# Optimization experiments

Measured on AMD Instinct MI355X. Metric: run time of the kernel, lower is better.

The kernel has to match this reference:

```python
import jax, jax.numpy as jnp
import numpy as np

# grid_size buffer registered in __init__: [1, gx, gy, gz]
GRID = jnp.array([1.0, 0.1, 0.1, 0.1], dtype=jnp.float32)


def setup_inputs() -> dict:
    key = jax.random.key(0)
    k1, k2 = jax.random.split(key)
    N, B = 4_000_000, 8
    batch = jax.random.randint(k1, (N, 1), 0, B).astype(jnp.float32)
    xyz = jax.random.uniform(k2, (N, 3), minval=0.0, maxval=50.0)
    points = jnp.concatenate([batch, xyz], axis=1)  # [N, 4]
    return {"points": points}


def reference(points):
    N = points.shape[0]
    # bounding box (batch column padded by 0.5 so each integer batch id gets its own bin)
    start = points.min(axis=0).at[0].add(-0.5)  # [4]
    end = points.max(axis=0).at[0].add(0.5)     # [4]
    # per-dim voxel coordinates and linear cluster id (grid_cluster)
    coords = jnp.floor((points - start) / GRID).astype(jnp.int32)        # [N, 4]
    num_vox = jnp.floor((end - start) / GRID).astype(jnp.int32) + 1      # [4]
    strides = jnp.concatenate([jnp.ones((1,), jnp.int32), jnp.cumprod(num_vox[:-1])])
    cluster = (coords * strides).sum(axis=1)                             # [N] int32
    # sorted unique + inverse; pad to static size N for jit-compatibility
    _, inv = jnp.unique(cluster, size=N, fill_value=jnp.int32(-1), return_inverse=True)
    inv = inv.reshape(N)
    # scatter-mean of points into voxels (rows >= num_grids are zero padding)
    sums = jax.ops.segment_sum(points, inv, num_segments=N)              # [N, 4]
    counts = jax.ops.segment_sum(jnp.ones((N,), points.dtype), inv, num_segments=N)
    sampled_grids = sums / jnp.maximum(counts, 1.0)[:, None]
    return sampled_grids, inv
```

## Files before the change

kernel.cpp:

```cpp
#include <hip/hip_runtime.h>
#include <stdint.h>


#define BSHIFT   17
#define BVOX     (1u << BSHIFT)
#define BWORDS   (BVOX / 32)
#define NBUCK    8800u
#define UCAP     640
#define NBLK     512
#define MMBLK    512
#define GRID_B   1.0f
#define GRID_XYZ 0.1f

static inline size_t alignUp(size_t x, size_t a) { return (x + a - 1) & ~(a - 1); }

struct DerivedT { float s0, s1, s2, s3; int st1, st2, st3; };

__device__ __forceinline__ DerivedT derive(const float* mm) {
    DerivedT d;
    d.s0 = mm[0] - 0.5f; d.s1 = mm[1]; d.s2 = mm[2]; d.s3 = mm[3];
    float e0 = mm[4] + 0.5f;
    int nv0 = (int)floorf((e0    - d.s0) / GRID_B)   + 1;
    int nv1 = (int)floorf((mm[5] - d.s1) / GRID_XYZ) + 1;
    int nv2 = (int)floorf((mm[6] - d.s2) / GRID_XYZ) + 1;
    d.st1 = nv0; d.st2 = nv0 * nv1; d.st3 = nv0 * nv1 * nv2;
    return d;
}

__device__ __forceinline__ uint32_t clusterOf(float4 p, const DerivedT& d) {
    int c0 = (int)floorf((p.x - d.s0) / GRID_B);
    int c1 = (int)floorf((p.y - d.s1) / GRID_XYZ);
    int c2 = (int)floorf((p.z - d.s2) / GRID_XYZ);
    int c3 = (int)floorf((p.w - d.s3) / GRID_XYZ);
    uint32_t c = (uint32_t)(c0 + c1 * d.st1 + c2 * d.st2 + c3 * d.st3);
    const uint32_t cap = NBUCK * BVOX - 1u;
    return (c < cap) ? c : cap;
}

__global__ __launch_bounds__(256) void k_minmax_partial(const float4* __restrict__ pts, int n,
                                                        float* __restrict__ partial) {
    __shared__ float smn[4][4], smx[4][4];
    float mn0 = 3.4e38f, mn1 = 3.4e38f, mn2 = 3.4e38f, mn3 = 3.4e38f;
    float mx0 = -3.4e38f, mx1 = -3.4e38f, mx2 = -3.4e38f, mx3 = -3.4e38f;
    for (int i = blockIdx.x * blockDim.x + threadIdx.x; i < n; i += gridDim.x * blockDim.x) {
        float4 p = pts[i];
        mn0 = fminf(mn0, p.x); mx0 = fmaxf(mx0, p.x);
        mn1 = fminf(mn1, p.y); mx1 = fmaxf(mx1, p.y);
        mn2 = fminf(mn2, p.z); mx2 = fmaxf(mx2, p.z);
        mn3 = fminf(mn3, p.w); mx3 = fmaxf(mx3, p.w);
    }
    #pragma unroll
    for (int off = 32; off >= 1; off >>= 1) {
        mn0 = fminf(mn0, __shfl_xor(mn0, off)); mx0 = fmaxf(mx0, __shfl_xor(mx0, off));
        mn1 = fminf(mn1, __shfl_xor(mn1, off)); mx1 = fmaxf(mx1, __shfl_xor(mx1, off));
        mn2 = fminf(mn2, __shfl_xor(mn2, off)); mx2 = fmaxf(mx2, __shfl_xor(mx2, off));
        mn3 = fminf(mn3, __shfl_xor(mn3, off)); mx3 = fmaxf(mx3, __shfl_xor(mx3, off));
    }
    const int wave = threadIdx.x >> 6;
    if ((threadIdx.x & 63) == 0) {
        smn[wave][0] = mn0; smn[wave][1] = mn1; smn[wave][2] = mn2; smn[wave][3] = mn3;
        smx[wave][0] = mx0; smx[wave][1] = mx1; smx[wave][2] = mx2; smx[wave][3] = mx3;
    }
    __syncthreads();
    if (threadIdx.x == 0) {
        #pragma unroll
        for (int w = 1; w < 4; ++w) {
            smn[0][0] = fminf(smn[0][0], smn[w][0]); smx[0][0] = fmaxf(smx[0][0], smx[w][0]);
            smn[0][1] = fminf(smn[0][1], smn[w][1]); smx[0][1] = fmaxf(smx[0][1], smx[w][1]);
            smn[0][2] = fminf(smn[0][2], smn[w][2]); smx[0][2] = fmaxf(smx[0][2], smx[w][2]);
            smn[0][3] = fminf(smn[0][3], smn[w][3]); smx[0][3] = fmaxf(smx[0][3], smx[w][3]);
        }
        float* p = partial + (size_t)blockIdx.x * 8;
        p[0] = smn[0][0]; p[1] = smn[0][1]; p[2] = smn[0][2]; p[3] = smn[0][3];
        p[4] = smx[0][0]; p[5] = smx[0][1]; p[6] = smx[0][2]; p[7] = smx[0][3];
    }
}

__global__ __launch_bounds__(256) void k_minmax_final(const float* __restrict__ partial,
                                                      float* __restrict__ mm) {
    __shared__ float smn[4][4], smx[4][4];
    float mn0 = 3.4e38f, mn1 = 3.4e38f, mn2 = 3.4e38f, mn3 = 3.4e38f;
    float mx0 = -3.4e38f, mx1 = -3.4e38f, mx2 = -3.4e38f, mx3 = -3.4e38f;
    for (int b = threadIdx.x; b < MMBLK; b += 256) {
        const float* p = partial + (size_t)b * 8;
        mn0 = fminf(mn0, p[0]); mn1 = fminf(mn1, p[1]);
        mn2 = fminf(mn2, p[2]); mn3 = fminf(mn3, p[3]);
        mx0 = fmaxf(mx0, p[4]); mx1 = fmaxf(mx1, p[5]);
        mx2 = fmaxf(mx2, p[6]); mx3 = fmaxf(mx3, p[7]);
    }
    #pragma unroll
    for (int off = 32; off >= 1; off >>= 1) {
        mn0 = fminf(mn0, __shfl_xor(mn0, off)); mx0 = fmaxf(mx0, __shfl_xor(mx0, off));
        mn1 = fminf(mn1, __shfl_xor(mn1, off)); mx1 = fmaxf(mx1, __shfl_xor(mx1, off));
        mn2 = fminf(mn2, __shfl_xor(mn2, off)); mx2 = fmaxf(mx2, __shfl_xor(mx2, off));
        mn3 = fminf(mn3, __shfl_xor(mn3, off)); mx3 = fmaxf(mx3, __shfl_xor(mx3, off));
    }
    const int wave = threadIdx.x >> 6;
    if ((threadIdx.x & 63) == 0) {
        smn[wave][0] = mn0; smn[wave][1] = mn1; smn[wave][2] = mn2; smn[wave][3] = mn3;
        smx[wave][0] = mx0; smx[wave][1] = mx1; smx[wave][2] = mx2; smx[wave][3] = mx3;
    }
    __syncthreads();
    if (threadIdx.x == 0) {
        #pragma unroll
        for (int w = 1; w < 4; ++w) {
            smn[0][0] = fminf(smn[0][0], smn[w][0]); smx[0][0] = fmaxf(smx[0][0], smx[w][0]);
            smn[0][1] = fminf(smn[0][1], smn[w][1]); smx[0][1] = fmaxf(smx[0][1], smx[w][1]);
            smn[0][2] = fminf(smn[0][2], smn[w][2]); smx[0][2] = fmaxf(smx[0][2], smx[w][2]);
            smn[0][3] = fminf(smn[0][3], smn[w][3]); smx[0][3] = fmaxf(smx[0][3], smx[w][3]);
        }
        mm[0] = smn[0][0]; mm[1] = smn[0][1]; mm[2] = smn[0][2]; mm[3] = smn[0][3];
        mm[4] = smx[0][0]; mm[5] = smx[0][1]; mm[6] = smx[0][2]; mm[7] = smx[0][3];
    }
}

__global__ __launch_bounds__(256) void k_hist(const float4* __restrict__ pts, int n, int ch,
                                              const float* __restrict__ mm,
                                              uint32_t* __restrict__ hist) {
    __shared__ uint32_t h[NBUCK];
    DerivedT d = derive(mm);
    const int blk = blockIdx.x, t = threadIdx.x;
    for (int i = t; i < (int)NBUCK; i += 256) h[i] = 0;
    __syncthreads();
    const int s = blk * ch, e = min(n, s + ch);
    for (int i = s + t; i < e; i += 256) {
        uint32_t c = clusterOf(pts[i], d);
        atomicAdd(&h[c >> BSHIFT], 1u);
    }
    __syncthreads();
    uint32_t* row = hist + (size_t)blk * NBUCK;
    for (int i = t; i < (int)NBUCK; i += 256) row[i] = h[i];
}

__global__ __launch_bounds__(256) void k_total(const uint32_t* __restrict__ hist,
                                               uint32_t* __restrict__ tot) {
    int b = blockIdx.x * 256 + threadIdx.x;
    if (b >= (int)NBUCK) return;
    uint32_t s = 0;
    for (int blk = 0; blk < NBLK; ++blk) s += hist[(size_t)blk * NBUCK + b];
    tot[b] = s;
}

__global__ __launch_bounds__(1024) void k_scan(const uint32_t* __restrict__ in,
                                               uint32_t* __restrict__ out,
                                               uint32_t* __restrict__ totOut, int nb) {
    __shared__ uint32_t s[1024];
    const int t = threadIdx.x;
    const int ITEMS = 9;
    uint32_t v[ITEMS]; uint32_t tot = 0;
    const int base = t * ITEMS;
    #pragma unroll
    for (int k = 0; k < ITEMS; ++k) {
        int i = base + k;
        v[k] = (i < nb) ? in[i] : 0u;
        tot += v[k];
    }
    s[t] = tot;
    __syncthreads();
    for (int o = 1; o < 1024; o <<= 1) {
        uint32_t add = (t >= o) ? s[t - o] : 0u;
        __syncthreads();
        s[t] += add;
        __syncthreads();
    }
    uint32_t run = s[t] - tot;
    #pragma unroll
    for (int k = 0; k < ITEMS; ++k) {
        int i = base + k;
        if (i < nb) out[i] = run;
        run += v[k];
    }
    if (t == 1023) *totOut = run;
}

__global__ __launch_bounds__(256) void k_rowscan(const uint32_t* __restrict__ hist,
                                                 const uint32_t* __restrict__ bucketBase,
                                                 uint32_t* __restrict__ baseM) {
    int b = blockIdx.x * 256 + threadIdx.x;
    if (b >= (int)NBUCK) return;
    uint32_t run = bucketBase[b];
    for (int blk = 0; blk < NBLK; ++blk) {
        size_t o = (size_t)blk * NBUCK + b;
        uint32_t v = hist[o];
        baseM[o] = run;
        run += v;
    }
}

__global__ __launch_bounds__(256) void k_place(const float4* __restrict__ pts, int n, int ch,
                                               const float* __restrict__ mm,
                                               const uint32_t* __restrict__ baseM,
                                               uint4* __restrict__ rec) {
    __shared__ uint32_t cur[NBUCK];
    DerivedT d = derive(mm);
    const int blk = blockIdx.x, t = threadIdx.x;
    const uint32_t* row = baseM + (size_t)blk * NBUCK;
    for (int i = t; i < (int)NBUCK; i += 256) cur[i] = row[i];
    __syncthreads();
    const int s = blk * ch, e = min(n, s + ch);
    for (int base = s + t; base < e; base += 4 * 256) {
        float4 p[4]; uint32_t c[4]; int idx[4]; bool val[4];
        #pragma unroll
        for (int k = 0; k < 4; ++k) {
            int i = base + k * 256;
            val[k] = (i < e);
            idx[k] = val[k] ? i : (e - 1);
            p[k] = pts[idx[k]];
        }
        #pragma unroll
        for (int k = 0; k < 4; ++k) c[k] = clusterOf(p[k], d);
        #pragma unroll
        for (int k = 0; k < 4; ++k) {
            if (val[k]) {
                uint32_t dest = atomicAdd(&cur[c[k] >> BSHIFT], 1u);
                rec[(size_t)dest * 2]     = make_uint4(__float_as_uint(p[k].x), __float_as_uint(p[k].y),
                                                       __float_as_uint(p[k].z), __float_as_uint(p[k].w));
                rec[(size_t)dest * 2 + 1] = make_uint4(c[k], (uint32_t)idx[k], 0u, 0u);
            }
        }
    }
}

__global__ __launch_bounds__(256) void k_bucket_count(const uint32_t* __restrict__ bucketBase,
                                                      const uint32_t* __restrict__ tot,
                                                      const uint4* __restrict__ rec,
                                                      uint32_t* __restrict__ uniqueCnt) {
    __shared__ uint32_t bm[BWORDS];
    __shared__ uint32_t sred[256];
    const int b = blockIdx.x;
    const int t = threadIdx.x;
    uint32_t m = tot[b];
    if (m == 0) { if (t == 0) uniqueCnt[b] = 0; return; }
    #pragma unroll
    for (int k = 0; k < BWORDS / 256; ++k) bm[t + k * 256] = 0;
    __syncthreads();
    const size_t s = bucketBase[b];
    for (uint32_t j = t; j < m; j += 256) {
        uint4 meta = rec[(s + j) * 2 + 1];
        uint32_t lc = meta.x & (BVOX - 1u);
        atomicOr(&bm[lc >> 5], 1u << (lc & 31u));
    }
    __syncthreads();
    uint32_t acc = 0;
    #pragma unroll
    for (int k = 0; k < BWORDS / 256; ++k) acc += __popc(bm[t + k * 256]);
    sred[t] = acc;
    __syncthreads();
    for (int o = 128; o > 0; o >>= 1) {
        if (t < o) sred[t] += sred[t + o];
        __syncthreads();
    }
    if (t == 0) uniqueCnt[b] = sred[0];
}

__global__ __launch_bounds__(256) void k_zero_pad(float4* __restrict__ outGrid4,
                                                  const uint32_t* __restrict__ totU, int n) {
    const uint32_t t0 = *totU;
    for (uint32_t j = blockIdx.x * blockDim.x + threadIdx.x + t0; j < (uint32_t)n;
         j += gridDim.x * blockDim.x) {
        outGrid4[j] = make_float4(0.f, 0.f, 0.f, 0.f);
    }
}

__global__ __launch_bounds__(256) void k_bucket_emit(const uint32_t* __restrict__ bucketBase,
                                                     const uint32_t* __restrict__ tot,
                                                     const uint4* __restrict__ rec,
                                                     const uint32_t* __restrict__ rankBase,
                                                     float4* __restrict__ outGrid4,
                                                     float* __restrict__ outInv) {
    __shared__ uint32_t bm[BWORDS];
    __shared__ uint16_t wpre[BWORDS];
    __shared__ float    s0[UCAP], s1[UCAP], s2[UCAP], s3[UCAP];
    __shared__ uint32_t cn[UCAP];
    __shared__ uint32_t sred[256];
    __shared__ uint32_t sU;
    const int b = blockIdx.x;
    const int t = threadIdx.x;
    uint32_t m = tot[b];
    if (m == 0) return;
    #pragma unroll
    for (int k = 0; k < BWORDS / 256; ++k) bm[t + k * 256] = 0;
    for (int u = t; u < UCAP; u += 256) { s0[u] = 0.f; s1[u] = 0.f; s2[u] = 0.f; s3[u] = 0.f; cn[u] = 0u; }
    __syncthreads();
    const size_t s = bucketBase[b];
    for (uint32_t j = t; j < m; j += 256) {
        uint4 meta = rec[(s + j) * 2 + 1];
        uint32_t lc = meta.x & (BVOX - 1u);
        atomicOr(&bm[lc >> 5], 1u << (lc & 31u));
    }
    __syncthreads();
    uint32_t wc[16]; uint32_t tt = 0;
    #pragma unroll
    for (int k = 0; k < 16; ++k) { wc[k] = __popc(bm[t * 16 + k]); tt += wc[k]; }
    sred[t] = tt;
    __syncthreads();
    for (int o = 1; o < 256; o <<= 1) {
        uint32_t add = (t >= o) ? sred[t - o] : 0u;
        __syncthreads();
        sred[t] += add;
        __syncthreads();
    }
    uint32_t run = sred[t] - tt;
    #pragma unroll
    for (int k = 0; k < 16; ++k) { wpre[t * 16 + k] = (uint16_t)run; run += wc[k]; }
    if (t == 255) sU = sred[255];
    __syncthreads();
    const uint32_t rb = rankBase[b];
    for (uint32_t j = t; j < m; j += 256) {
        uint4 pw   = rec[(s + j) * 2];
        uint4 meta = rec[(s + j) * 2 + 1];
        uint32_t lc  = meta.x & (BVOX - 1u);
        uint32_t w   = lc >> 5, bit = lc & 31u;
        uint32_t lr  = wpre[w] + __popc(bm[w] & ((1u << bit) - 1u));
        if (lr >= UCAP) lr = UCAP - 1u;
        atomicAdd(&s0[lr], __uint_as_float(pw.x));
        atomicAdd(&s1[lr], __uint_as_float(pw.y));
        atomicAdd(&s2[lr], __uint_as_float(pw.z));
        atomicAdd(&s3[lr], __uint_as_float(pw.w));
        atomicAdd(&cn[lr], 1u);
        outInv[meta.y] = (float)(rb + lr);
    }
    __syncthreads();
    uint32_t U = sU; if (U > UCAP) U = UCAP;
    for (uint32_t u = t; u < U; u += 256) {
        float fc = (float)cn[u];
        float4 o;
        o.x = s0[u] / fc; o.y = s1[u] / fc; o.z = s2[u] / fc; o.w = s3[u] / fc;
        outGrid4[rb + u] = o;
    }
}

extern "C" void kernel_launch(void* const* d_in, const int* in_sizes, int n_in,
                              void* d_out, int out_size, void* d_ws, size_t ws_size,
                              hipStream_t stream) {
    const float4* pts = (const float4*)d_in[0];
    const int n = in_sizes[0] / 4;
    const int ch = (n + NBLK - 1) / NBLK;

    char* ws = (char*)d_ws;
    size_t off = 0;
    uint32_t* hist       = (uint32_t*)(ws + off); off += alignUp((size_t)NBLK * NBUCK * 4, 256);
    uint32_t* baseM      = (uint32_t*)(ws + off); off += alignUp((size_t)NBLK * NBUCK * 4, 256);
    uint4*    rec        = (uint4*)   (ws + off); off += alignUp((size_t)n * 32, 256);
    uint32_t* tot        = (uint32_t*)(ws + off); off += alignUp((size_t)NBUCK * 4, 256);
    uint32_t* bucketBase = (uint32_t*)(ws + off); off += alignUp((size_t)NBUCK * 4, 256);
    uint32_t* uniqueCnt  = (uint32_t*)(ws + off); off += alignUp((size_t)NBUCK * 4, 256);
    uint32_t* rankBase   = (uint32_t*)(ws + off); off += alignUp((size_t)NBUCK * 4, 256);
    float*    partial    = (float*)   (ws + off); off += alignUp((size_t)MMBLK * 8 * 4, 256);
    uint32_t* totU       = (uint32_t*)(ws + off); off += 256;
    uint32_t* totPts     = (uint32_t*)(ws + off); off += 256;
    float*    mm         = (float*)   (ws + off); off += 256;

    float* outGrid = (float*)d_out;
    float* outInv  = outGrid + (size_t)n * 4;

    const int NB256 = ((int)NBUCK + 255) / 256;

    k_minmax_partial<<<MMBLK, 256, 0, stream>>>(pts, n, partial);
    k_minmax_final<<<1, 256, 0, stream>>>(partial, mm);
    k_hist<<<NBLK, 256, 0, stream>>>(pts, n, ch, mm, hist);
    k_total<<<NB256, 256, 0, stream>>>(hist, tot);
    k_scan<<<1, 1024, 0, stream>>>(tot, bucketBase, totPts, (int)NBUCK);
    k_rowscan<<<NB256, 256, 0, stream>>>(hist, bucketBase, baseM);
    k_place<<<NBLK, 256, 0, stream>>>(pts, n, ch, mm, baseM, rec);
    k_bucket_count<<<(int)NBUCK, 256, 0, stream>>>(bucketBase, tot, rec, uniqueCnt);
    k_scan<<<1, 1024, 0, stream>>>(uniqueCnt, rankBase, totU, (int)NBUCK);
    k_zero_pad<<<256, 256, 0, stream>>>((float4*)outGrid, totU, n);
    k_bucket_emit<<<(int)NBUCK, 256, 0, stream>>>(bucketBase, tot, rec, rankBase,
                                                  (float4*)outGrid, outInv);
}
```

Before: 443.9 us.

## Compute local voxel ranks once in count pass and reuse them in emit

The count kernel now builds each bucket's occupancy bitmap, runs a wave-shuffle prefix scan, and writes a 16-bit local rank per record to a new workspace array. The emit kernel reads that rank instead of rebuilding the bitmap and redoing a serial shared-memory scan, which removes a full pass over the record metadata plus many barriers. The per-block histogram is also stored as uint16, and the bucket-total reduction is split into eight segments so more blocks run in parallel. In exchange the change adds an n-sized uint16 array write and read, and the 16-bit histogram assumes no block puts more than 65535 points into one bucket.

After: 430.6 us. 3.0% less time.

```diff
diff --git a/kernel.cpp b/kernel.cpp
--- a/kernel.cpp
+++ b/kernel.cpp
@@ -8,6 +8,7 @@
 #define NBUCK    8800u
 #define UCAP     640
 #define NBLK     512
+#define SEG      8
 #define MMBLK    512
 #define GRID_B   1.0f
 #define GRID_XYZ 0.1f
@@ -116,7 +117,7 @@
 
 __global__ __launch_bounds__(256) void k_hist(const float4* __restrict__ pts, int n, int ch,
                                               const float* __restrict__ mm,
-                                              uint32_t* __restrict__ hist) {
+                                              uint16_t* __restrict__ hist) {
     __shared__ uint32_t h[NBUCK];
     DerivedT d = derive(mm);
     const int blk = blockIdx.x, t = threadIdx.x;
@@ -128,16 +129,28 @@
         atomicAdd(&h[c >> BSHIFT], 1u);
     }
     __syncthreads();
-    uint32_t* row = hist + (size_t)blk * NBUCK;
-    for (int i = t; i < (int)NBUCK; i += 256) row[i] = h[i];
-}
-
-__global__ __launch_bounds__(256) void k_total(const uint32_t* __restrict__ hist,
-                                               uint32_t* __restrict__ tot) {
+    uint16_t* row = hist + (size_t)blk * NBUCK;
+    for (int i = t; i < (int)NBUCK; i += 256) row[i] = (uint16_t)h[i];
+}
+
+__global__ __launch_bounds__(256) void k_total_part(const uint16_t* __restrict__ hist,
+                                                    uint32_t* __restrict__ totP, int nb256) {
+    const int seg  = blockIdx.x / nb256;
+    const int b    = (blockIdx.x % nb256) * 256 + threadIdx.x;
+    if (b >= (int)NBUCK) return;
+    uint32_t s = 0;
+    const int b0 = seg * (NBLK / SEG), b1 = b0 + (NBLK / SEG);
+    for (int blk = b0; blk < b1; ++blk) s += hist[(size_t)blk * NBUCK + b];
+    totP[(size_t)seg * NBUCK + b] = s;
+}
+
+__global__ __launch_bounds__(256) void k_total_red(const uint32_t* __restrict__ totP,
+                                                   uint32_t* __restrict__ tot) {
     int b = blockIdx.x * 256 + threadIdx.x;
     if (b >= (int)NBUCK) return;
     uint32_t s = 0;
-    for (int blk = 0; blk < NBLK; ++blk) s += hist[(size_t)blk * NBUCK + b];
+    #pragma unroll
+    for (int seg = 0; seg < SEG; ++seg) s += totP[(size_t)seg * NBUCK + b];
     tot[b] = s;
 }
 
@@ -173,7 +186,7 @@
     if (t == 1023) *totOut = run;
 }
 
-__global__ __launch_bounds__(256) void k_rowscan(const uint32_t* __restrict__ hist,
+__global__ __launch_bounds__(256) void k_rowscan(const uint16_t* __restrict__ hist,
                                                  const uint32_t* __restrict__ bucketBase,
                                                  uint32_t* __restrict__ baseM) {
     int b = blockIdx.x * 256 + threadIdx.x;
@@ -224,9 +237,11 @@
 __global__ __launch_bounds__(256) void k_bucket_count(const uint32_t* __restrict__ bucketBase,
                                                       const uint32_t* __restrict__ tot,
                                                       const uint4* __restrict__ rec,
-                                                      uint32_t* __restrict__ uniqueCnt) {
+                                                      uint32_t* __restrict__ uniqueCnt,
+                                                      uint16_t* __restrict__ lrS) {
     __shared__ uint32_t bm[BWORDS];
-    __shared__ uint32_t sred[256];
+    __shared__ uint16_t wpre[BWORDS];
+    __shared__ uint32_t wtot[4];
     const int b = blockIdx.x;
     const int t = threadIdx.x;
     uint32_t m = tot[b];
@@ -236,21 +251,36 @@
     __syncthreads();
     const size_t s = bucketBase[b];
     for (uint32_t j = t; j < m; j += 256) {
-        uint4 meta = rec[(s + j) * 2 + 1];
-        uint32_t lc = meta.x & (BVOX - 1u);
+        uint32_t lc = rec[(s + j) * 2 + 1].x & (BVOX - 1u);
         atomicOr(&bm[lc >> 5], 1u << (lc & 31u));
     }
     __syncthreads();
-    uint32_t acc = 0;
-    #pragma unroll
-    for (int k = 0; k < BWORDS / 256; ++k) acc += __popc(bm[t + k * 256]);
-    sred[t] = acc;
-    __syncthreads();
-    for (int o = 128; o > 0; o >>= 1) {
-        if (t < o) sred[t] += sred[t + o];
-        __syncthreads();
-    }
-    if (t == 0) uniqueCnt[b] = sred[0];
+    uint32_t wc[16]; uint32_t tt = 0;
+    #pragma unroll
+    for (int k = 0; k < 16; ++k) { wc[k] = __popc(bm[t * 16 + k]); tt += wc[k]; }
+    uint32_t incl = tt;
+    #pragma unroll
+    for (int o = 1; o < 64; o <<= 1) {
+        uint32_t v = __shfl_up(incl, o);
+        if ((t & 63) >= o) incl += v;
+    }
+    if ((t & 63) == 63) wtot[t >> 6] = incl;
+    __syncthreads();
+    uint32_t wpref = 0;
+    #pragma unroll
+    for (int w = 0; w < 4; ++w) wpref += (w < (t >> 6)) ? wtot[w] : 0u;
+    uint32_t run = wpref + incl - tt;
+    #pragma unroll
+    for (int k = 0; k < 16; ++k) { wpre[t * 16 + k] = (uint16_t)run; run += wc[k]; }
+    if (t == 255) uniqueCnt[b] = run;
+    __syncthreads();
+    for (uint32_t j = t; j < m; j += 256) {
+        uint32_t lc  = rec[(s + j) * 2 + 1].x & (BVOX - 1u);
+        uint32_t w   = lc >> 5, bit = lc & 31u;
+        uint32_t lr  = wpre[w] + __popc(bm[w] & ((1u << bit) - 1u));
+        if (lr >= UCAP) lr = UCAP - 1u;
+        lrS[s + j] = (uint16_t)lr;
+    }
 }
 
 __global__ __launch_bounds__(256) void k_zero_pad(float4* __restrict__ outGrid4,
@@ -264,55 +294,26 @@
 
 __global__ __launch_bounds__(256) void k_bucket_emit(const uint32_t* __restrict__ bucketBase,
                                                      const uint32_t* __restrict__ tot,
+                                                     const uint32_t* __restrict__ uniqueCnt,
                                                      const uint4* __restrict__ rec,
+                                                     const uint16_t* __restrict__ lrS,
                                                      const uint32_t* __restrict__ rankBase,
                                                      float4* __restrict__ outGrid4,
                                                      float* __restrict__ outInv) {
-    __shared__ uint32_t bm[BWORDS];
-    __shared__ uint16_t wpre[BWORDS];
     __shared__ float    s0[UCAP], s1[UCAP], s2[UCAP], s3[UCAP];
     __shared__ uint32_t cn[UCAP];
-    __shared__ uint32_t sred[256];
-    __shared__ uint32_t sU;
     const int b = blockIdx.x;
     const int t = threadIdx.x;
     uint32_t m = tot[b];
     if (m == 0) return;
-    #pragma unroll
-    for (int k = 0; k < BWORDS / 256; ++k) bm[t + k * 256] = 0;
     for (int u = t; u < UCAP; u += 256) { s0[u] = 0.f; s1[u] = 0.f; s2[u] = 0.f; s3[u] = 0.f; cn[u] = 0u; }
     __syncthreads();
     const size_t s = bucketBase[b];
-    for (uint32_t j = t; j < m; j += 256) {
-        uint4 meta = rec[(s + j) * 2 + 1];
-        uint32_t lc = meta.x & (BVOX - 1u);
-        atomicOr(&bm[lc >> 5], 1u << (lc & 31u));
-    }
-    __syncthreads();
-    uint32_t wc[16]; uint32_t tt = 0;
-    #pragma unroll
-    for (int k = 0; k < 16; ++k) { wc[k] = __popc(bm[t * 16 + k]); tt += wc[k]; }
-    sred[t] = tt;
-    __syncthreads();
-    for (int o = 1; o < 256; o <<= 1) {
-        uint32_t add = (t >= o) ? sred[t - o] : 0u;
-        __syncthreads();
-        sred[t] += add;
-        __syncthreads();
-    }
-    uint32_t run = sred[t] - tt;
-    #pragma unroll
-    for (int k = 0; k < 16; ++k) { wpre[t * 16 + k] = (uint16_t)run; run += wc[k]; }
-    if (t == 255) sU = sred[255];
-    __syncthreads();
     const uint32_t rb = rankBase[b];
     for (uint32_t j = t; j < m; j += 256) {
         uint4 pw   = rec[(s + j) * 2];
         uint4 meta = rec[(s + j) * 2 + 1];
-        uint32_t lc  = meta.x & (BVOX - 1u);
-        uint32_t w   = lc >> 5, bit = lc & 31u;
-        uint32_t lr  = wpre[w] + __popc(bm[w] & ((1u << bit) - 1u));
-        if (lr >= UCAP) lr = UCAP - 1u;
+        uint32_t lr = lrS[s + j];
         atomicAdd(&s0[lr], __uint_as_float(pw.x));
         atomicAdd(&s1[lr], __uint_as_float(pw.y));
         atomicAdd(&s2[lr], __uint_as_float(pw.z));
@@ -321,7 +322,7 @@
         outInv[meta.y] = (float)(rb + lr);
     }
     __syncthreads();
-    uint32_t U = sU; if (U > UCAP) U = UCAP;
+    uint32_t U = uniqueCnt[b]; if (U > UCAP) U = UCAP;
     for (uint32_t u = t; u < U; u += 256) {
         float fc = (float)cn[u];
         float4 o;
@@ -339,9 +340,11 @@
 
     char* ws = (char*)d_ws;
     size_t off = 0;
-    uint32_t* hist       = (uint32_t*)(ws + off); off += alignUp((size_t)NBLK * NBUCK * 4, 256);
+    uint16_t* hist       = (uint16_t*)(ws + off); off += alignUp((size_t)NBLK * NBUCK * 2, 256);
     uint32_t* baseM      = (uint32_t*)(ws + off); off += alignUp((size_t)NBLK * NBUCK * 4, 256);
     uint4*    rec        = (uint4*)   (ws + off); off += alignUp((size_t)n * 32, 256);
+    uint16_t* lrS        = (uint16_t*)(ws + off); off += alignUp((size_t)n * 2, 256);
+    uint32_t* totP       = (uint32_t*)(ws + off); off += alignUp((size_t)SEG * NBUCK * 4, 256);
     uint32_t* tot        = (uint32_t*)(ws + off); off += alignUp((size_t)NBUCK * 4, 256);
     uint32_t* bucketBase = (uint32_t*)(ws + off); off += alignUp((size_t)NBUCK * 4, 256);
     uint32_t* uniqueCnt  = (uint32_t*)(ws + off); off += alignUp((size_t)NBUCK * 4, 256);
@@ -359,13 +362,14 @@
     k_minmax_partial<<<MMBLK, 256, 0, stream>>>(pts, n, partial);
     k_minmax_final<<<1, 256, 0, stream>>>(partial, mm);
     k_hist<<<NBLK, 256, 0, stream>>>(pts, n, ch, mm, hist);
-    k_total<<<NB256, 256, 0, stream>>>(hist, tot);
+    k_total_part<<<NB256 * SEG, 256, 0, stream>>>(hist, totP, NB256);
+    k_total_red<<<NB256, 256, 0, stream>>>(totP, tot);
     k_scan<<<1, 1024, 0, stream>>>(tot, bucketBase, totPts, (int)NBUCK);
     k_rowscan<<<NB256, 256, 0, stream>>>(hist, bucketBase, baseM);
     k_place<<<NBLK, 256, 0, stream>>>(pts, n, ch, mm, baseM, rec);
-    k_bucket_count<<<(int)NBUCK, 256, 0, stream>>>(bucketBase, tot, rec, uniqueCnt);
+    k_bucket_count<<<(int)NBUCK, 256, 0, stream>>>(bucketBase, tot, rec, uniqueCnt, lrS);
     k_scan<<<1, 1024, 0, stream>>>(uniqueCnt, rankBase, totU, (int)NBUCK);
     k_zero_pad<<<256, 256, 0, stream>>>((float4*)outGrid, totU, n);
-    k_bucket_emit<<<(int)NBUCK, 256, 0, stream>>>(bucketBase, tot, rec, rankBase,
-                                                  (float4*)outGrid, outInv);
-}
+    k_bucket_emit<<<(int)NBUCK, 256, 0, stream>>>(bucketBase, tot, uniqueCnt, rec, lrS,
+                                                  rankBase, (float4*)outGrid, outInv);
+}
```
